# Kernel tuning notes

Measured on AMD Instinct MI355X. Metric: run time of the kernel, lower is better.

## Reference

```python
import jax, jax.numpy as jnp
import numpy as np

N = 30000      # nodes
E = 480000     # edges (avg degree 16)
NF = 4         # n_field
NM = 8         # n_meshfield
H = 128        # hidden_size == latent_size
T = 4          # n_time
DEPTH_MID = 8  # depth-2 middle convs per GCNBlock
EPS = 1e-5     # PyG InstanceNorm eps
DT = 5 * (4.0 / 200)  # = 0.1, hard-coded in forward


def _glorot(k, shape):
    fan_in = shape[-2]
    return (jax.random.uniform(k, shape, jnp.float32, -1.0, 1.0) / np.sqrt(fan_in)).astype(jnp.float32)


def setup_inputs() -> dict:
    key = jax.random.key(0)
    ks = jax.random.split(key, 12)
    inp = {}
    inp['F_0'] = jax.random.normal(ks[0], (N, NF), jnp.float32)
    inp['edge_index'] = jax.random.randint(ks[1], (2, E), 0, N)
    inp['meshfield'] = jax.random.normal(ks[2], (N, NM), jnp.float32)
    inp['n_time'] = T
    # mesh_decriptor GCNBlock params (10 GCNConv layers)
    inp['mesh_W0'] = _glorot(ks[3], (NM, H)); inp['mesh_b0'] = jnp.zeros((H,), jnp.float32)
    inp['mesh_Wh'] = _glorot(ks[4], (DEPTH_MID, H, H)); inp['mesh_bh'] = jnp.zeros((DEPTH_MID, H), jnp.float32)
    inp['mesh_W9'] = _glorot(ks[5], (H, H)); inp['mesh_b9'] = jnp.zeros((H,), jnp.float32)
    # differentiator GCNBlock params; input dim = n_field + latent_size
    din = NF + H
    inp['diff_W0'] = _glorot(ks[6], (din, H)); inp['diff_b0'] = jnp.zeros((H,), jnp.float32)
    inp['diff_Wh'] = _glorot(ks[7], (DEPTH_MID, H, H)); inp['diff_bh'] = jnp.zeros((DEPTH_MID, H), jnp.float32)
    inp['diff_W9'] = _glorot(ks[8], (H, NF)); inp['diff_b9'] = jnp.zeros((NF,), jnp.float32)
    return inp


def _gcn_norm(edge_index, n):
    # PyG GCNConv: add self-loops, sym-normalize D^-1/2 (A+I) D^-1/2
    loops = jnp.arange(n)
    row = jnp.concatenate([edge_index[0], loops])
    col = jnp.concatenate([edge_index[1], loops])
    deg = jax.ops.segment_sum(jnp.ones_like(col, jnp.float32), col, num_segments=n)
    dinv = jnp.where(deg > 0, jax.lax.rsqrt(jnp.maximum(deg, 1.0)), 0.0)
    return row, col, dinv[row] * dinv[col]


def _conv(x, W, b, row, col, enorm, n):
    h = x @ W                                   # [n, out]
    m = h[row] * enorm[:, None]                 # gather + edge normalization
    return jax.ops.segment_sum(m, col, num_segments=n) + b  # scatter-add + bias


def _instance_norm(x):
    # single graph, affine=False: per-channel normalize over nodes
    m = x.mean(axis=0)
    v = x.var(axis=0)
    return (x - m) * jax.lax.rsqrt(v + EPS)


def _gcn_block(x, W0, b0, Wh, bh, W9, b9, row, col, enorm, n):
    x = _conv(x, W0, b0, row, col, enorm, n)
    x = _instance_norm(x)
    def body(c, wb):
        W, b = wb
        return _conv(jax.nn.relu(c), W, b, row, col, enorm, n), None
    x, _ = jax.lax.scan(body, x, (Wh, bh))
    return _conv(x, W9, b9, row, col, enorm, n)


def reference(F_0, edge_index, meshfield, n_time,
              mesh_W0, mesh_b0, mesh_Wh, mesh_bh, mesh_W9, mesh_b9,
              diff_W0, diff_b0, diff_Wh, diff_bh, diff_W9, diff_b9):
    n = F_0.shape[0]
    row, col, enorm = _gcn_norm(edge_index, n)
    mesh = jnp.tanh(_gcn_block(meshfield, mesh_W0, mesh_b0, mesh_Wh, mesh_bh,
                               mesh_W9, mesh_b9, row, col, enorm, n))

    def step(F_cur, _):
        x = jnp.concatenate([F_cur, mesh], axis=1)   # [n, n_field + latent]
        F_dot = jnp.tanh(_gcn_block(x, diff_W0, diff_b0, diff_Wh, diff_bh,
                                    diff_W9, diff_b9, row, col, enorm, n))
        F_next = jnp.tanh(F_cur + F_dot * DT)
        # original: F_current = F_next.detach()
        return jax.lax.stop_gradient(F_next), (F_next, F_dot)

    _, (Fs, F_dots) = jax.lax.scan(step, F_0, None, length=n_time)
    # [T, n, f] -> [n, T, f] to match torch.cat(..., dim=1)
    return jnp.transpose(Fs, (1, 0, 2)), jnp.transpose(F_dots, (1, 0, 2))
```

## Files before the change

### kernel.cpp

```cpp
#include <hip/hip_runtime.h>
#include <math.h>

typedef __attribute__((ext_vector_type(8))) short short8;
typedef __attribute__((ext_vector_type(4))) float f32x4;
typedef unsigned int uint;
typedef unsigned short ushort;

__device__ __forceinline__ ushort f2bf(float f) {
  union { float f; uint u; } v; v.f = f;
  uint u = v.u;
  uint r = (u + 0x7FFFu + ((u >> 16) & 1u)) >> 16;
  return (ushort)r;
}
__device__ __forceinline__ float bflo(uint u) { union { uint u; float f; } v; v.u = u << 16; return v.f; }
__device__ __forceinline__ float bfhi(uint u) { union { uint u; float f; } v; v.u = u & 0xFFFF0000u; return v.f; }
__device__ __forceinline__ uint packbf(float a, float b) { return (uint)f2bf(a) | ((uint)f2bf(b) << 16); }


static __global__ void k_count(const int* __restrict__ col, int* __restrict__ cnt, int E) {
  int e = blockIdx.x * blockDim.x + threadIdx.x;
  if (e < E) atomicAdd(&cnt[col[e]], 1);
}

static __global__ void k_dinv(const int* __restrict__ cnt, float* __restrict__ dinv, int N) {
  int v = blockIdx.x * blockDim.x + threadIdx.x;
  if (v < N) dinv[v] = rsqrtf((float)cnt[v] + 1.0f);
}

static __global__ void k_scan(const int* __restrict__ cnt, int* __restrict__ rowptr, int N) {
  __shared__ int buf[1024];
  __shared__ int carry;
  int t = threadIdx.x;
  if (t == 0) carry = 0;
  __syncthreads();
  for (int base = 0; base < N; base += 1024) {
    int i = base + t;
    int x = (i < N) ? cnt[i] : 0;
    buf[t] = x;
    __syncthreads();
    for (int o = 1; o < 1024; o <<= 1) {
      int val = (t >= o) ? buf[t - o] : 0;
      __syncthreads();
      buf[t] += val;
      __syncthreads();
    }
    int inc = buf[t];
    if (i < N) rowptr[i] = carry + inc - x;
    __syncthreads();
    if (t == 1023) carry += inc;
    __syncthreads();
  }
  if (t == 0) rowptr[N] = carry;
}

static __global__ void k_fill(const int* __restrict__ row, const int* __restrict__ col,
                              const float* __restrict__ dinv, const int* __restrict__ rowptr,
                              int* __restrict__ fillc, int* __restrict__ csr_src,
                              float* __restrict__ csr_w, int E) {
  int e = blockIdx.x * blockDim.x + threadIdx.x;
  if (e >= E) return;
  int s = row[e], d = col[e];
  int pos = rowptr[d] + atomicAdd(&fillc[d], 1);
  csr_src[pos] = s;
  csr_w[pos] = dinv[s] * dinv[d];
}


static __global__ void k_wprep(const float* __restrict__ W, ushort* __restrict__ Wt,
                               int K, int Kpad, int Nc) {
  int l = blockIdx.y;
  int idx = blockIdx.x * 256 + threadIdx.x;
  if (idx >= Nc * Kpad) return;
  int n = idx / Kpad, k = idx - n * Kpad;
  const float* Wl = W + (size_t)l * K * Nc;
  ushort* Wtl = Wt + (size_t)l * Nc * Kpad;
  Wtl[idx] = (k < K) ? f2bf(Wl[(size_t)k * Nc + n]) : (ushort)0;
}


static __global__ __launch_bounds__(256) void k_gemm16(
    const ushort* __restrict__ A, const ushort* __restrict__ Bt,
    ushort* __restrict__ Y, int M, int K) {
  __shared__ ushort As[128 * 40];
  __shared__ ushort Bs[128 * 40];
  const int tid = threadIdx.x;
  const int lane = tid & 63;
  const int wave = tid >> 6;
  const int wr = wave >> 1, wc = wave & 1;
  const int bm = blockIdx.x * 128;
  const int l15 = lane & 15, lk = lane >> 4;
  const int r0 = tid >> 2, o0 = tid & 3;

  f32x4 acc[4][4];
#pragma unroll
  for (int i = 0; i < 4; ++i)
#pragma unroll
    for (int j = 0; j < 4; ++j) acc[i][j] = (f32x4){0.f, 0.f, 0.f, 0.f};

  for (int k0 = 0; k0 < K; k0 += 32) {
    short8 a0 = *(const short8*)(A + (size_t)(bm + r0) * K + k0 + o0 * 8);
    short8 a1 = *(const short8*)(A + (size_t)(bm + r0 + 64) * K + k0 + o0 * 8);
    short8 b0 = *(const short8*)(Bt + (size_t)r0 * K + k0 + o0 * 8);
    short8 b1 = *(const short8*)(Bt + (size_t)(r0 + 64) * K + k0 + o0 * 8);
    __syncthreads();
    *(short8*)(As + r0 * 40 + o0 * 8) = a0;
    *(short8*)(As + (r0 + 64) * 40 + o0 * 8) = a1;
    *(short8*)(Bs + r0 * 40 + o0 * 8) = b0;
    *(short8*)(Bs + (r0 + 64) * 40 + o0 * 8) = b1;
    __syncthreads();
    short8 af[4], bfr[4];
#pragma unroll
    for (int i = 0; i < 4; ++i) {
      af[i]  = *(const short8*)(As + (wr * 64 + i * 16 + l15) * 40 + lk * 8);
      bfr[i] = *(const short8*)(Bs + (wc * 64 + i * 16 + l15) * 40 + lk * 8);
    }
#pragma unroll
    for (int i = 0; i < 4; ++i)
#pragma unroll
      for (int j = 0; j < 4; ++j)
        acc[i][j] = __builtin_amdgcn_mfma_f32_16x16x32_bf16(af[i], bfr[j], acc[i][j], 0, 0, 0);
  }
#pragma unroll
  for (int i = 0; i < 4; ++i) {
#pragma unroll
    for (int r = 0; r < 4; ++r) {
      int row = bm + wr * 64 + i * 16 + lk * 4 + r;
      if (row < M) {
#pragma unroll
        for (int j = 0; j < 4; ++j) {
          int col = wc * 64 + j * 16 + l15;
          Y[(size_t)row * 128 + col] = f2bf(acc[i][j][r]);
        }
      }
    }
  }
}


static __global__ __launch_bounds__(256) void k_gemm_small(
    const ushort* __restrict__ A, const float* __restrict__ W, float* __restrict__ Y, int M) {
  __shared__ float Ws[512];
  int tid = threadIdx.x;
  for (int i = tid; i < 512; i += 256) Ws[i] = W[i];
  __syncthreads();
  int m = blockIdx.x * 256 + tid;
  if (m >= M) return;
  const uint* a = (const uint*)(A + (size_t)m * 128);
  float a0 = 0, a1 = 0, a2 = 0, a3 = 0;
#pragma unroll 8
  for (int k2 = 0; k2 < 64; ++k2) {
    uint u = a[k2];
    float x0 = bflo(u), x1 = bfhi(u);
    const float* w = Ws + k2 * 8;
    a0 += x0 * w[0] + x1 * w[4];
    a1 += x0 * w[1] + x1 * w[5];
    a2 += x0 * w[2] + x1 * w[6];
    a3 += x0 * w[3] + x1 * w[7];
  }
  float* y = Y + (size_t)m * 4;
  y[0] = a0; y[1] = a1; y[2] = a2; y[3] = a3;
}


static __global__ __launch_bounds__(256) void k_agg16(
    const ushort* __restrict__ Hm, const int* __restrict__ rowptr,
    const int* __restrict__ csr_src, const float* __restrict__ csr_w,
    const float* __restrict__ dinv, const float* __restrict__ bias,
    float* __restrict__ outF, int actF,
    ushort* __restrict__ outB, int reluB,
    int N) {
  int node = blockIdx.x * 4 + (threadIdx.x >> 6);
  if (node >= N) return;
  int lane = threadIdx.x & 63;
  const uint* __restrict__ Hu = (const uint*)Hm;
  float dv = dinv[node];
  float w = dv * dv;
  uint su = Hu[(size_t)node * 64 + lane];
  float acc0 = w * bflo(su), acc1 = w * bfhi(su);
  int s = rowptr[node], e = rowptr[node + 1];
  int i = s;
  for (; i + 4 <= e; i += 4) {
    int s0 = csr_src[i], s1 = csr_src[i + 1], s2 = csr_src[i + 2], s3 = csr_src[i + 3];
    float w0 = csr_w[i], w1 = csr_w[i + 1], w2 = csr_w[i + 2], w3 = csr_w[i + 3];
    uint u0 = Hu[(size_t)s0 * 64 + lane];
    uint u1 = Hu[(size_t)s1 * 64 + lane];
    uint u2 = Hu[(size_t)s2 * 64 + lane];
    uint u3 = Hu[(size_t)s3 * 64 + lane];
    acc0 += w0 * bflo(u0) + w1 * bflo(u1) + w2 * bflo(u2) + w3 * bflo(u3);
    acc1 += w0 * bfhi(u0) + w1 * bfhi(u1) + w2 * bfhi(u2) + w3 * bfhi(u3);
  }
  for (; i < e; ++i) {
    int s0 = csr_src[i];
    float w0 = csr_w[i];
    uint u0 = Hu[(size_t)s0 * 64 + lane];
    acc0 += w0 * bflo(u0);
    acc1 += w0 * bfhi(u0);
  }
  float2 bb = *(const float2*)(bias + lane * 2);
  acc0 += bb.x; acc1 += bb.y;
  if (outF) {
    float o0 = acc0, o1 = acc1;
    if (actF == 2) { o0 = tanhf(o0); o1 = tanhf(o1); }
    *(float2*)(outF + (size_t)node * 128 + lane * 2) = make_float2(o0, o1);
  }
  if (outB) {
    float o0 = acc0, o1 = acc1;
    if (reluB) { o0 = fmaxf(o0, 0.f); o1 = fmaxf(o1, 0.f); }
    ((uint*)outB)[(size_t)node * 64 + lane] = packbf(o0, o1);
  }
}


static __global__ void k_agg_f32(const float* __restrict__ Hm, float* __restrict__ Y,
                                 const int* __restrict__ rowptr, const int* __restrict__ csr_src,
                                 const float* __restrict__ csr_w, const float* __restrict__ dinv,
                                 const float* __restrict__ bias, int N, int C) {
  int idx = blockIdx.x * blockDim.x + threadIdx.x;
  if (idx >= N * C) return;
  int v = idx / C, c = idx - v * C;
  float dv = dinv[v];
  float acc = dv * dv * Hm[(size_t)v * C + c];
  int s = rowptr[v], e = rowptr[v + 1];
  for (int i = s; i < e; ++i) acc += csr_w[i] * Hm[(size_t)csr_src[i] * C + c];
  Y[idx] = acc + bias[c];
}


static __global__ __launch_bounds__(256) void k_in_part(const float* __restrict__ X,
                                                        float* __restrict__ acc, int N) {
  int tid = threadIdx.x;
  int c4 = (tid & 31) * 4;
  int rsub = tid >> 5;
  int row0 = blockIdx.x * 512 + rsub;
  int rowEnd = min(blockIdx.x * 512 + 512, N);
  float s0 = 0, s1 = 0, s2 = 0, s3 = 0, q0 = 0, q1 = 0, q2 = 0, q3 = 0;
  for (int r = row0; r < rowEnd; r += 8) {
    float4 v = *(const float4*)(X + (size_t)r * 128 + c4);
    s0 += v.x; s1 += v.y; s2 += v.z; s3 += v.w;
    q0 += v.x * v.x; q1 += v.y * v.y; q2 += v.z * v.z; q3 += v.w * v.w;
  }
  __shared__ float sb[8][132], qb[8][132];
  sb[rsub][c4] = s0; sb[rsub][c4 + 1] = s1; sb[rsub][c4 + 2] = s2; sb[rsub][c4 + 3] = s3;
  qb[rsub][c4] = q0; qb[rsub][c4 + 1] = q1; qb[rsub][c4 + 2] = q2; qb[rsub][c4 + 3] = q3;
  __syncthreads();
  if (tid < 128) {
    float ss = 0, qq = 0;
#pragma unroll
    for (int g = 0; g < 8; ++g) { ss += sb[g][tid]; qq += qb[g][tid]; }
    atomicAdd(&acc[tid], ss);
    atomicAdd(&acc[128 + tid], qq);
  }
}

static __global__ void k_in_fin(const float* __restrict__ acc, float* __restrict__ meanv,
                                float* __restrict__ scalev, int N) {
  int c = threadIdx.x;
  if (c < 128) {
    float m = acc[c] / (float)N;
    float var = acc[128 + c] / (float)N - m * m;
    meanv[c] = m;
    scalev[c] = rsqrtf(var + 1e-5f);
  }
}

static __global__ void k_in_apply(const float* __restrict__ X, const float* __restrict__ meanv,
                                  const float* __restrict__ scalev, ushort* __restrict__ outB, int N) {
  int idx = blockIdx.x * blockDim.x + threadIdx.x;
  if (idx >= N * 64) return;
  int c2 = idx & 63;
  float2 x = *(const float2*)(X + (size_t)idx * 2);
  float2 mm = *(const float2*)(meanv + c2 * 2);
  float2 sc = *(const float2*)(scalev + c2 * 2);
  float o0 = fmaxf((x.x - mm.x) * sc.x, 0.f);
  float o1 = fmaxf((x.y - mm.y) * sc.y, 0.f);
  ((uint*)outB)[idx] = packbf(o0, o1);
}


static __global__ void k_cast_mesh0(const float* __restrict__ MF, ushort* __restrict__ A16, int N) {
  int idx = blockIdx.x * blockDim.x + threadIdx.x;
  if (idx >= N * 16) return;
  int v = idx >> 4, c2 = idx & 15;
  int c = c2 * 2;
  float x0 = 0.f, x1 = 0.f;
  if (c < 8) { x0 = MF[v * 8 + c]; x1 = MF[v * 8 + c + 1]; }
  ((uint*)A16)[idx] = packbf(x0, x1);
}

static __global__ void k_concat16(const float* __restrict__ F, const float* __restrict__ meshL,
                                  ushort* __restrict__ A16, int N) {
  int idx = blockIdx.x * blockDim.x + threadIdx.x;
  if (idx >= N * 80) return;
  int v = idx / 80, c2 = idx - v * 80;
  int c = c2 * 2;
  float x0 = 0.f, x1 = 0.f;
  if (c < 4) { x0 = F[v * 4 + c]; x1 = F[v * 4 + c + 1]; }
  else if (c < 132) { float2 m = *(const float2*)(meshL + (size_t)v * 128 + (c - 4)); x0 = m.x; x1 = m.y; }
  ((uint*)A16)[idx] = packbf(x0, x1);
}

static __global__ void k_copy(const float* __restrict__ A, float* __restrict__ B, int n) {
  int i = blockIdx.x * blockDim.x + threadIdx.x;
  if (i < n) B[i] = A[i];
}

static __global__ void k_step_finish(const float* __restrict__ fdot_pre,
                                     const float* __restrict__ Fcur, float* __restrict__ Fnext,
                                     float* __restrict__ out, int N, int T, int t) {
  int idx = blockIdx.x * blockDim.x + threadIdx.x;
  if (idx >= N * 4) return;
  int v = idx >> 2, f = idx & 3;
  float fd = tanhf(fdot_pre[idx]);
  float fn = tanhf(Fcur[idx] + fd * 0.1f);
  Fnext[idx] = fn;
  out[((size_t)v * T + t) * 4 + f] = fn;
  out[(size_t)N * T * 4 + ((size_t)v * T + t) * 4 + f] = fd;
}


extern "C" void kernel_launch(void* const* d_in, const int* in_sizes, int n_in,
                              void* d_out, int out_size, void* d_ws, size_t ws_size,
                              hipStream_t stream) {
  const float* F0        = (const float*)d_in[0];
  const int*   ei        = (const int*)d_in[1];
  const float* meshfield = (const float*)d_in[2];
  const float* mesh_W0 = (const float*)d_in[4];
  const float* mesh_b0 = (const float*)d_in[5];
  const float* mesh_Wh = (const float*)d_in[6];
  const float* mesh_bh = (const float*)d_in[7];
  const float* mesh_W9 = (const float*)d_in[8];
  const float* mesh_b9 = (const float*)d_in[9];
  const float* diff_W0 = (const float*)d_in[10];
  const float* diff_b0 = (const float*)d_in[11];
  const float* diff_Wh = (const float*)d_in[12];
  const float* diff_bh = (const float*)d_in[13];
  const float* diff_W9 = (const float*)d_in[14];
  const float* diff_b9 = (const float*)d_in[15];

  const int N = in_sizes[0] / 4;
  const int E = in_sizes[1] / 2;
  const int H = in_sizes[5];
  const int T = out_size / (N * 4 * 2);
  const int DEPTH = in_sizes[7] / H;
  const int Mpad = (N + 127) / 128 * 128;
  const int DIN_K = 160;

  const int* erow = ei;
  const int* ecol = ei + E;

  char* p = (char*)d_ws;
  auto alloc = [&](size_t bytes) { char* r = p; p += (bytes + 255) & ~(size_t)255; return r; };
  float* dinv   = (float*)alloc((size_t)N * 4);
  float* X      = (float*)alloc((size_t)N * H * 4);
  float* meshL  = (float*)alloc((size_t)N * H * 4);
  ushort* A16   = (ushort*)alloc((size_t)Mpad * DIN_K * 2);
  ushort* Msg16 = (ushort*)alloc((size_t)Mpad * H * 2);
  float* msg4   = (float*)alloc((size_t)N * 4 * 4);
  float* fdotp  = (float*)alloc((size_t)N * 4 * 4);
  float* fcur0  = (float*)alloc((size_t)N * 4 * 4);
  float* fcur1  = (float*)alloc((size_t)N * 4 * 4);
  float* statac = (float*)alloc(256 * 4);
  float* meanv  = (float*)alloc(128 * 4);
  float* scalev = (float*)alloc(128 * 4);
  ushort* W0t_m = (ushort*)alloc((size_t)128 * 32 * 2);
  ushort* Wht_m = (ushort*)alloc((size_t)DEPTH * 128 * 128 * 2);
  ushort* W9t_m = (ushort*)alloc((size_t)128 * 128 * 2);
  ushort* W0t_d = (ushort*)alloc((size_t)128 * 160 * 2);
  ushort* Wht_d = (ushort*)alloc((size_t)DEPTH * 128 * 128 * 2);
  float* csr_w  = (float*)alloc((size_t)E * 4);
  int* cnt      = (int*)alloc((size_t)N * 4);
  int* rowptr   = (int*)alloc((size_t)(N + 1) * 4);
  int* fillc    = (int*)alloc((size_t)N * 4);
  int* csr_src  = (int*)alloc((size_t)E * 4);

  {
    dim3 g0((128 * 32 + 255) / 256, 1);
    k_wprep<<<g0, 256, 0, stream>>>(mesh_W0, W0t_m, 8, 32, 128);
    dim3 gh((128 * 128 + 255) / 256, DEPTH);
    k_wprep<<<gh, 256, 0, stream>>>(mesh_Wh, Wht_m, 128, 128, 128);
    dim3 g9((128 * 128 + 255) / 256, 1);
    k_wprep<<<g9, 256, 0, stream>>>(mesh_W9, W9t_m, 128, 128, 128);
    dim3 gd((128 * 160 + 255) / 256, 1);
    k_wprep<<<gd, 256, 0, stream>>>(diff_W0, W0t_d, 132, 160, 128);
    k_wprep<<<gh, 256, 0, stream>>>(diff_Wh, Wht_d, 128, 128, 128);
  }

  hipMemsetAsync(cnt, 0, (size_t)N * 4, stream);
  hipMemsetAsync(fillc, 0, (size_t)N * 4, stream);
  k_count<<<(E + 255) / 256, 256, 0, stream>>>(ecol, cnt, E);
  k_dinv<<<(N + 255) / 256, 256, 0, stream>>>(cnt, dinv, N);
  k_scan<<<1, 1024, 0, stream>>>(cnt, rowptr, N);
  k_fill<<<(E + 255) / 256, 256, 0, stream>>>(erow, ecol, dinv, rowptr, fillc, csr_src, csr_w, E);

  auto gemm = [&](const ushort* A, const ushort* Bt, int K) {
    k_gemm16<<<Mpad / 128, 256, 0, stream>>>(A, Bt, Msg16, N, K);
  };
  auto agg = [&](const float* bias, float* outF, int actF, ushort* outB, int reluB) {
    k_agg16<<<(N + 3) / 4, 256, 0, stream>>>(Msg16, rowptr, csr_src, csr_w, dinv, bias,
                                             outF, actF, outB, reluB, N);
  };
  auto instnorm = [&]() {
    hipMemsetAsync(statac, 0, 256 * 4, stream);
    k_in_part<<<(N + 511) / 512, 256, 0, stream>>>(X, statac, N);
    k_in_fin<<<1, 128, 0, stream>>>(statac, meanv, scalev, N);
    k_in_apply<<<(N * 64 + 255) / 256, 256, 0, stream>>>(X, meanv, scalev, A16, N);
  };

  k_cast_mesh0<<<(N * 16 + 255) / 256, 256, 0, stream>>>(meshfield, A16, N);
  gemm(A16, W0t_m, 32);
  agg(mesh_b0, X, 0, nullptr, 0);
  instnorm();
  for (int i = 0; i < DEPTH; ++i) {
    gemm(A16, Wht_m + (size_t)i * 128 * 128, 128);
    agg(mesh_bh + (size_t)i * H, nullptr, 0, A16, (i < DEPTH - 1) ? 1 : 0);
  }
  gemm(A16, W9t_m, 128);
  agg(mesh_b9, meshL, 2 , nullptr, 0);

  k_copy<<<(N * 4 + 255) / 256, 256, 0, stream>>>(F0, fcur0, N * 4);
  float* fc = fcur0;
  float* fn = fcur1;
  float* out = (float*)d_out;

  for (int t = 0; t < T; ++t) {
    k_concat16<<<(N * 80 + 255) / 256, 256, 0, stream>>>(fc, meshL, A16, N);
    gemm(A16, W0t_d, DIN_K);
    agg(diff_b0, X, 0, nullptr, 0);
    instnorm();
    for (int i = 0; i < DEPTH; ++i) {
      gemm(A16, Wht_d + (size_t)i * 128 * 128, 128);
      agg(diff_bh + (size_t)i * H, nullptr, 0, A16, (i < DEPTH - 1) ? 1 : 0);
    }
    k_gemm_small<<<(N + 255) / 256, 256, 0, stream>>>(A16, diff_W9, msg4, N);
    k_agg_f32<<<(N * 4 + 255) / 256, 256, 0, stream>>>(msg4, fdotp, rowptr, csr_src, csr_w,
                                                       dinv, diff_b9, N, 4);
    k_step_finish<<<(N * 4 + 255) / 256, 256, 0, stream>>>(fdotp, fc, fn, out, N, T, t);
    float* tmp = fc; fc = fn; fn = tmp;
  }
}
```

Before: 2.092 ms.

## Fuse neighbor aggregation into GEMM conv kernel using aggregate-then-transform order

Each GCN conv layer becomes one kernel. It first aggregates neighbor features (A·X) for a 128-node tile into LDS, then multiplies by the weight with MFMA and applies bias and activation in the epilogue. This relies on (A·X)·W = A·(X·W) and removes the intermediate message buffer round trip and one launch per layer. The cost is a serial gather phase per block with low parallelism: only 235 blocks, each wave handling 32 nodes in sequence. Gathering 160-wide inputs for the first diff layer also costs more. The single-block scan now uses shuffle-based chunked scanning. Instance-norm statistics are reduced through per-block partials instead of atomics, which drops a memset.

```diff
diff --git a/kernel.cpp b/kernel.cpp
--- a/kernel.cpp
+++ b/kernel.cpp
@@ -27,30 +27,39 @@
   if (v < N) dinv[v] = rsqrtf((float)cnt[v] + 1.0f);
 }
 
-static __global__ void k_scan(const int* __restrict__ cnt, int* __restrict__ rowptr, int N) {
-  __shared__ int buf[1024];
-  __shared__ int carry;
-  int t = threadIdx.x;
-  if (t == 0) carry = 0;
+static __global__ __launch_bounds__(1024) void k_scan(const int* __restrict__ cnt,
+                                                      int* __restrict__ rowptr, int N) {
+  const int t = threadIdx.x;
+  const int per = (N + 1023) / 1024;
+  int lo = t * per, hi = min(lo + per, N);
+  if (lo > N) lo = N;
+  if (hi < lo) hi = lo;
+  int sum = 0;
+  for (int i = lo; i < hi; ++i) sum += cnt[i];
+  int lane = t & 63, w = t >> 6;
+  int v = sum;
+#pragma unroll
+  for (int d = 1; d < 64; d <<= 1) {
+    int u = __shfl_up(v, d, 64);
+    if (lane >= d) v += u;
+  }
+  __shared__ int wsum[16];
+  if (lane == 63) wsum[w] = v;
   __syncthreads();
-  for (int base = 0; base < N; base += 1024) {
-    int i = base + t;
-    int x = (i < N) ? cnt[i] : 0;
-    buf[t] = x;
-    __syncthreads();
-    for (int o = 1; o < 1024; o <<= 1) {
-      int val = (t >= o) ? buf[t - o] : 0;
-      __syncthreads();
-      buf[t] += val;
-      __syncthreads();
-    }
-    int inc = buf[t];
-    if (i < N) rowptr[i] = carry + inc - x;
-    __syncthreads();
-    if (t == 1023) carry += inc;
-    __syncthreads();
-  }
-  if (t == 0) rowptr[N] = carry;
+  if (t < 16) {
+    int x = wsum[t];
+#pragma unroll
+    for (int d = 1; d < 16; d <<= 1) {
+      int u = __shfl_up(x, d, 64);
+      if (t >= d) x += u;
+    }
+    wsum[t] = x;
+  }
+  __syncthreads();
+  int base = (w ? wsum[w - 1] : 0) + v - sum;
+  int run = base;
+  for (int i = lo; i < hi; ++i) { rowptr[i] = run; run += cnt[i]; }
+  if (t == 1023) rowptr[N] = run;
 }
 
 static __global__ void k_fill(const int* __restrict__ row, const int* __restrict__ col,
@@ -78,41 +87,120 @@
 }
 
 
-static __global__ __launch_bounds__(256) void k_gemm16(
-    const ushort* __restrict__ A, const ushort* __restrict__ Bt,
-    ushort* __restrict__ Y, int M, int K) {
-  __shared__ ushort As[128 * 40];
-  __shared__ ushort Bs[128 * 40];
+template <int KPAD>
+static __global__ __launch_bounds__(256) void k_conv(
+    const ushort* __restrict__ Xin, const ushort* __restrict__ Bt,
+    const int* __restrict__ rowptr, const int* __restrict__ csr_src,
+    const float* __restrict__ csr_w, const float* __restrict__ dinv,
+    const float* __restrict__ bias,
+    float* __restrict__ outF, int actF,
+    ushort* __restrict__ outB, int reluB,
+    int N) {
+  constexpr int KU = KPAD / 2;
+  constexpr int STR = KPAD + 8;
+  constexpr int STRU = STR / 2;
+  constexpr int K8 = KPAD / 8;
+  __shared__ ushort As[128 * STR];
+  __shared__ ushort Bs[128 * STR];
   const int tid = threadIdx.x;
   const int lane = tid & 63;
   const int wave = tid >> 6;
+  const int bm = blockIdx.x * 128;
+
+  for (int ii = tid; ii < 128 * K8; ii += 256) {
+    int r = ii / K8, o = ii - r * K8;
+    *(short8*)(Bs + r * STR + o * 8) = *(const short8*)(Bt + (size_t)r * KPAD + o * 8);
+  }
+
+  const uint* __restrict__ Xu = (const uint*)Xin;
+  uint* AsU = (uint*)As;
+
+  if constexpr (KU <= 64) {
+    constexpr int NPI = 64 / KU;
+    const int c = lane % KU;
+    const int sub = lane / KU;
+    for (int j = wave * 32 + sub; j < (wave + 1) * 32; j += NPI) {
+      int nd = bm + j;
+      float a0 = 0.f, a1 = 0.f;
+      if (nd < N) {
+        float dv = dinv[nd];
+        float wsl = dv * dv;
+        uint u = Xu[(size_t)nd * KU + c];
+        a0 = wsl * bflo(u);
+        a1 = wsl * bfhi(u);
+        int s = rowptr[nd], e = rowptr[nd + 1];
+        int i = s;
+        for (; i + 4 <= e; i += 4) {
+          int s0 = csr_src[i], s1 = csr_src[i + 1], s2 = csr_src[i + 2], s3 = csr_src[i + 3];
+          float w0 = csr_w[i], w1 = csr_w[i + 1], w2 = csr_w[i + 2], w3 = csr_w[i + 3];
+          uint u0 = Xu[(size_t)s0 * KU + c];
+          uint u1 = Xu[(size_t)s1 * KU + c];
+          uint u2 = Xu[(size_t)s2 * KU + c];
+          uint u3 = Xu[(size_t)s3 * KU + c];
+          a0 += w0 * bflo(u0) + w1 * bflo(u1) + w2 * bflo(u2) + w3 * bflo(u3);
+          a1 += w0 * bfhi(u0) + w1 * bfhi(u1) + w2 * bfhi(u2) + w3 * bfhi(u3);
+        }
+        for (; i < e; ++i) {
+          float w0 = csr_w[i];
+          uint u0 = Xu[(size_t)csr_src[i] * KU + c];
+          a0 += w0 * bflo(u0);
+          a1 += w0 * bfhi(u0);
+        }
+      }
+      AsU[j * STRU + c] = packbf(a0, a1);
+    }
+  } else {
+    for (int j = wave * 32; j < (wave + 1) * 32; ++j) {
+      int nd = bm + j;
+      float a0 = 0.f, a1 = 0.f, b0 = 0.f, b1 = 0.f;
+      const int c0 = lane, c1 = lane + 64;
+      const bool has2 = lane < (KU - 64);
+      if (nd < N) {
+        float dv = dinv[nd];
+        float wsl = dv * dv;
+        uint u = Xu[(size_t)nd * KU + c0];
+        a0 = wsl * bflo(u);
+        a1 = wsl * bfhi(u);
+        if (has2) {
+          uint u2 = Xu[(size_t)nd * KU + c1];
+          b0 = wsl * bflo(u2);
+          b1 = wsl * bfhi(u2);
+        }
+        int s = rowptr[nd], e = rowptr[nd + 1];
+        for (int i = s; i < e; ++i) {
+          int sv = csr_src[i];
+          float w0 = csr_w[i];
+          uint u0 = Xu[(size_t)sv * KU + c0];
+          a0 += w0 * bflo(u0);
+          a1 += w0 * bfhi(u0);
+          if (has2) {
+            uint u2 = Xu[(size_t)sv * KU + c1];
+            b0 += w0 * bflo(u2);
+            b1 += w0 * bfhi(u2);
+          }
+        }
+      }
+      AsU[j * STRU + c0] = packbf(a0, a1);
+      if (has2) AsU[j * STRU + c1] = packbf(b0, b1);
+    }
+  }
+  __syncthreads();
+
   const int wr = wave >> 1, wc = wave & 1;
-  const int bm = blockIdx.x * 128;
   const int l15 = lane & 15, lk = lane >> 4;
-  const int r0 = tid >> 2, o0 = tid & 3;
-
   f32x4 acc[4][4];
 #pragma unroll
   for (int i = 0; i < 4; ++i)
 #pragma unroll
     for (int j = 0; j < 4; ++j) acc[i][j] = (f32x4){0.f, 0.f, 0.f, 0.f};
 
-  for (int k0 = 0; k0 < K; k0 += 32) {
-    short8 a0 = *(const short8*)(A + (size_t)(bm + r0) * K + k0 + o0 * 8);
-    short8 a1 = *(const short8*)(A + (size_t)(bm + r0 + 64) * K + k0 + o0 * 8);
-    short8 b0 = *(const short8*)(Bt + (size_t)r0 * K + k0 + o0 * 8);
-    short8 b1 = *(const short8*)(Bt + (size_t)(r0 + 64) * K + k0 + o0 * 8);
-    __syncthreads();
-    *(short8*)(As + r0 * 40 + o0 * 8) = a0;
-    *(short8*)(As + (r0 + 64) * 40 + o0 * 8) = a1;
-    *(short8*)(Bs + r0 * 40 + o0 * 8) = b0;
-    *(short8*)(Bs + (r0 + 64) * 40 + o0 * 8) = b1;
-    __syncthreads();
+#pragma unroll
+  for (int k0 = 0; k0 < KPAD; k0 += 32) {
     short8 af[4], bfr[4];
 #pragma unroll
     for (int i = 0; i < 4; ++i) {
-      af[i]  = *(const short8*)(As + (wr * 64 + i * 16 + l15) * 40 + lk * 8);
-      bfr[i] = *(const short8*)(Bs + (wc * 64 + i * 16 + l15) * 40 + lk * 8);
+      af[i]  = *(const short8*)(As + (wr * 64 + i * 16 + l15) * STR + k0 + lk * 8);
+      bfr[i] = *(const short8*)(Bs + (wc * 64 + i * 16 + l15) * STR + k0 + lk * 8);
     }
 #pragma unroll
     for (int i = 0; i < 4; ++i)
@@ -120,16 +208,22 @@
       for (int j = 0; j < 4; ++j)
         acc[i][j] = __builtin_amdgcn_mfma_f32_16x16x32_bf16(af[i], bfr[j], acc[i][j], 0, 0, 0);
   }
+
 #pragma unroll
   for (int i = 0; i < 4; ++i) {
 #pragma unroll
     for (int r = 0; r < 4; ++r) {
       int row = bm + wr * 64 + i * 16 + lk * 4 + r;
-      if (row < M) {
-#pragma unroll
-        for (int j = 0; j < 4; ++j) {
-          int col = wc * 64 + j * 16 + l15;
-          Y[(size_t)row * 128 + col] = f2bf(acc[i][j][r]);
+      if (row >= N) continue;
+#pragma unroll
+      for (int j = 0; j < 4; ++j) {
+        int col = wc * 64 + j * 16 + l15;
+        float v = acc[i][j][r] + bias[col];
+        if (outF) {
+          outF[(size_t)row * 128 + col] = (actF == 2) ? tanhf(v) : v;
+        }
+        if (outB) {
+          outB[(size_t)row * 128 + col] = f2bf(reluB ? fmaxf(v, 0.f) : v);
         }
       }
     }
@@ -162,55 +256,6 @@
 }
 
 
-static __global__ __launch_bounds__(256) void k_agg16(
-    const ushort* __restrict__ Hm, const int* __restrict__ rowptr,
-    const int* __restrict__ csr_src, const float* __restrict__ csr_w,
-    const float* __restrict__ dinv, const float* __restrict__ bias,
-    float* __restrict__ outF, int actF,
-    ushort* __restrict__ outB, int reluB,
-    int N) {
-  int node = blockIdx.x * 4 + (threadIdx.x >> 6);
-  if (node >= N) return;
-  int lane = threadIdx.x & 63;
-  const uint* __restrict__ Hu = (const uint*)Hm;
-  float dv = dinv[node];
-  float w = dv * dv;
-  uint su = Hu[(size_t)node * 64 + lane];
-  float acc0 = w * bflo(su), acc1 = w * bfhi(su);
-  int s = rowptr[node], e = rowptr[node + 1];
-  int i = s;
-  for (; i + 4 <= e; i += 4) {
-    int s0 = csr_src[i], s1 = csr_src[i + 1], s2 = csr_src[i + 2], s3 = csr_src[i + 3];
-    float w0 = csr_w[i], w1 = csr_w[i + 1], w2 = csr_w[i + 2], w3 = csr_w[i + 3];
-    uint u0 = Hu[(size_t)s0 * 64 + lane];
-    uint u1 = Hu[(size_t)s1 * 64 + lane];
-    uint u2 = Hu[(size_t)s2 * 64 + lane];
-    uint u3 = Hu[(size_t)s3 * 64 + lane];
-    acc0 += w0 * bflo(u0) + w1 * bflo(u1) + w2 * bflo(u2) + w3 * bflo(u3);
-    acc1 += w0 * bfhi(u0) + w1 * bfhi(u1) + w2 * bfhi(u2) + w3 * bfhi(u3);
-  }
-  for (; i < e; ++i) {
-    int s0 = csr_src[i];
-    float w0 = csr_w[i];
-    uint u0 = Hu[(size_t)s0 * 64 + lane];
-    acc0 += w0 * bflo(u0);
-    acc1 += w0 * bfhi(u0);
-  }
-  float2 bb = *(const float2*)(bias + lane * 2);
-  acc0 += bb.x; acc1 += bb.y;
-  if (outF) {
-    float o0 = acc0, o1 = acc1;
-    if (actF == 2) { o0 = tanhf(o0); o1 = tanhf(o1); }
-    *(float2*)(outF + (size_t)node * 128 + lane * 2) = make_float2(o0, o1);
-  }
-  if (outB) {
-    float o0 = acc0, o1 = acc1;
-    if (reluB) { o0 = fmaxf(o0, 0.f); o1 = fmaxf(o1, 0.f); }
-    ((uint*)outB)[(size_t)node * 64 + lane] = packbf(o0, o1);
-  }
-}
-
-
 static __global__ void k_agg_f32(const float* __restrict__ Hm, float* __restrict__ Y,
                                  const int* __restrict__ rowptr, const int* __restrict__ csr_src,
                                  const float* __restrict__ csr_w, const float* __restrict__ dinv,
@@ -227,7 +272,7 @@
 
 
 static __global__ __launch_bounds__(256) void k_in_part(const float* __restrict__ X,
-                                                        float* __restrict__ acc, int N) {
+                                                        float* __restrict__ partial, int N) {
   int tid = threadIdx.x;
   int c4 = (tid & 31) * 4;
   int rsub = tid >> 5;
@@ -247,20 +292,24 @@
     float ss = 0, qq = 0;
 #pragma unroll
     for (int g = 0; g < 8; ++g) { ss += sb[g][tid]; qq += qb[g][tid]; }
-    atomicAdd(&acc[tid], ss);
-    atomicAdd(&acc[128 + tid], qq);
-  }
-}
-
-static __global__ void k_in_fin(const float* __restrict__ acc, float* __restrict__ meanv,
-                                float* __restrict__ scalev, int N) {
+    partial[(size_t)blockIdx.x * 256 + tid] = ss;
+    partial[(size_t)blockIdx.x * 256 + 128 + tid] = qq;
+  }
+}
+
+static __global__ void k_in_fin(const float* __restrict__ partial, int NB,
+                                float* __restrict__ meanv, float* __restrict__ scalev, int N) {
   int c = threadIdx.x;
-  if (c < 128) {
-    float m = acc[c] / (float)N;
-    float var = acc[128 + c] / (float)N - m * m;
-    meanv[c] = m;
-    scalev[c] = rsqrtf(var + 1e-5f);
-  }
+  if (c >= 128) return;
+  float s = 0, q = 0;
+  for (int b = 0; b < NB; ++b) {
+    s += partial[(size_t)b * 256 + c];
+    q += partial[(size_t)b * 256 + 128 + c];
+  }
+  float m = s / (float)N;
+  float var = q / (float)N - m * m;
+  meanv[c] = m;
+  scalev[c] = rsqrtf(var + 1e-5f);
 }
 
 static __global__ void k_in_apply(const float* __restrict__ X, const float* __restrict__ meanv,
@@ -277,18 +326,18 @@
 }
 
 
-static __global__ void k_cast_mesh0(const float* __restrict__ MF, ushort* __restrict__ A16, int N) {
+static __global__ void k_cast_mesh0(const float* __restrict__ MF, ushort* __restrict__ C32, int N) {
   int idx = blockIdx.x * blockDim.x + threadIdx.x;
   if (idx >= N * 16) return;
   int v = idx >> 4, c2 = idx & 15;
   int c = c2 * 2;
   float x0 = 0.f, x1 = 0.f;
   if (c < 8) { x0 = MF[v * 8 + c]; x1 = MF[v * 8 + c + 1]; }
-  ((uint*)A16)[idx] = packbf(x0, x1);
+  ((uint*)C32)[idx] = packbf(x0, x1);
 }
 
 static __global__ void k_concat16(const float* __restrict__ F, const float* __restrict__ meshL,
-                                  ushort* __restrict__ A16, int N) {
+                                  ushort* __restrict__ C160, int N) {
   int idx = blockIdx.x * blockDim.x + threadIdx.x;
   if (idx >= N * 80) return;
   int v = idx / 80, c2 = idx - v * 80;
@@ -296,7 +345,7 @@
   float x0 = 0.f, x1 = 0.f;
   if (c < 4) { x0 = F[v * 4 + c]; x1 = F[v * 4 + c + 1]; }
   else if (c < 132) { float2 m = *(const float2*)(meshL + (size_t)v * 128 + (c - 4)); x0 = m.x; x1 = m.y; }
-  ((uint*)A16)[idx] = packbf(x0, x1);
+  ((uint*)C160)[idx] = packbf(x0, x1);
 }
 
 static __global__ void k_copy(const float* __restrict__ A, float* __restrict__ B, int n) {
@@ -343,7 +392,7 @@
   const int T = out_size / (N * 4 * 2);
   const int DEPTH = in_sizes[7] / H;
   const int Mpad = (N + 127) / 128 * 128;
-  const int DIN_K = 160;
+  const int NB_IN = (N + 511) / 512;
 
   const int* erow = ei;
   const int* ecol = ei + E;
@@ -353,13 +402,15 @@
   float* dinv   = (float*)alloc((size_t)N * 4);
   float* X      = (float*)alloc((size_t)N * H * 4);
   float* meshL  = (float*)alloc((size_t)N * H * 4);
-  ushort* A16   = (ushort*)alloc((size_t)Mpad * DIN_K * 2);
-  ushort* Msg16 = (ushort*)alloc((size_t)Mpad * H * 2);
+  ushort* C32   = (ushort*)alloc((size_t)Mpad * 32 * 2);
+  ushort* C160  = (ushort*)alloc((size_t)Mpad * 160 * 2);
+  ushort* X16a  = (ushort*)alloc((size_t)Mpad * 128 * 2);
+  ushort* X16b  = (ushort*)alloc((size_t)Mpad * 128 * 2);
   float* msg4   = (float*)alloc((size_t)N * 4 * 4);
   float* fdotp  = (float*)alloc((size_t)N * 4 * 4);
   float* fcur0  = (float*)alloc((size_t)N * 4 * 4);
   float* fcur1  = (float*)alloc((size_t)N * 4 * 4);
-  float* statac = (float*)alloc(256 * 4);
+  float* partial= (float*)alloc((size_t)NB_IN * 256 * 4);
   float* meanv  = (float*)alloc(128 * 4);
   float* scalev = (float*)alloc(128 * 4);
   ushort* W0t_m = (ushort*)alloc((size_t)128 * 32 * 2);
@@ -392,30 +443,38 @@
   k_scan<<<1, 1024, 0, stream>>>(cnt, rowptr, N);
   k_fill<<<(E + 255) / 256, 256, 0, stream>>>(erow, ecol, dinv, rowptr, fillc, csr_src, csr_w, E);
 
-  auto gemm = [&](const ushort* A, const ushort* Bt, int K) {
-    k_gemm16<<<Mpad / 128, 256, 0, stream>>>(A, Bt, Msg16, N, K);
+  const int GCONV = Mpad / 128;
+
+  auto conv32 = [&](const ushort* Xin, const ushort* Bt, const float* b,
+                    float* oF, int aF, ushort* oB, int rB) {
+    k_conv<32><<<GCONV, 256, 0, stream>>>(Xin, Bt, rowptr, csr_src, csr_w, dinv, b, oF, aF, oB, rB, N);
   };
-  auto agg = [&](const float* bias, float* outF, int actF, ushort* outB, int reluB) {
-    k_agg16<<<(N + 3) / 4, 256, 0, stream>>>(Msg16, rowptr, csr_src, csr_w, dinv, bias,
-                                             outF, actF, outB, reluB, N);
+  auto conv128 = [&](const ushort* Xin, const ushort* Bt, const float* b,
+                     float* oF, int aF, ushort* oB, int rB) {
+    k_conv<128><<<GCONV, 256, 0, stream>>>(Xin, Bt, rowptr, csr_src, csr_w, dinv, b, oF, aF, oB, rB, N);
+  };
+  auto conv160 = [&](const ushort* Xin, const ushort* Bt, const float* b,
+                     float* oF, int aF, ushort* oB, int rB) {
+    k_conv<160><<<GCONV, 256, 0, stream>>>(Xin, Bt, rowptr, csr_src, csr_w, dinv, b, oF, aF, oB, rB, N);
   };
   auto instnorm = [&]() {
-    hipMemsetAsync(statac, 0, 256 * 4, stream);
-    k_in_part<<<(N + 511) / 512, 256, 0, stream>>>(X, statac, N);
-    k_in_fin<<<1, 128, 0, stream>>>(statac, meanv, scalev, N);
-    k_in_apply<<<(N * 64 + 255) / 256, 256, 0, stream>>>(X, meanv, scalev, A16, N);
+    k_in_part<<<NB_IN, 256, 0, stream>>>(X, partial, N);
+    k_in_fin<<<1, 128, 0, stream>>>(partial, NB_IN, meanv, scalev, N);
+    k_in_apply<<<(N * 64 + 255) / 256, 256, 0, stream>>>(X, meanv, scalev, X16a, N);
   };
 
-  k_cast_mesh0<<<(N * 16 + 255) / 256, 256, 0, stream>>>(meshfield, A16, N);
-  gemm(A16, W0t_m, 32);
-  agg(mesh_b0, X, 0, nullptr, 0);
+  k_cast_mesh0<<<(N * 16 + 255) / 256, 256, 0, stream>>>(meshfield, C32, N);
+  conv32(C32, W0t_m, mesh_b0, X, 0, nullptr, 0);
   instnorm();
-  for (int i = 0; i < DEPTH; ++i) {
-    gemm(A16, Wht_m + (size_t)i * 128 * 128, 128);
-    agg(mesh_bh + (size_t)i * H, nullptr, 0, A16, (i < DEPTH - 1) ? 1 : 0);
-  }
-  gemm(A16, W9t_m, 128);
-  agg(mesh_b9, meshL, 2 , nullptr, 0);
+  {
+    ushort* cur = X16a; ushort* nxt = X16b;
+    for (int i = 0; i < DEPTH; ++i) {
+      conv128(cur, Wht_m + (size_t)i * 128 * 128, mesh_bh + (size_t)i * H,
+              nullptr, 0, nxt, (i < DEPTH - 1) ? 1 : 0);
+      ushort* tmp = cur; cur = nxt; nxt = tmp;
+    }
+    conv128(cur, W9t_m, mesh_b9, meshL, 2 , nullptr, 0);
+  }
 
   k_copy<<<(N * 4 + 255) / 256, 256, 0, stream>>>(F0, fcur0, N * 4);
   float* fc = fcur0;
@@ -423,15 +482,16 @@
   float* out = (float*)d_out;
 
   for (int t = 0; t < T; ++t) {
-    k_concat16<<<(N * 80 + 255) / 256, 256, 0, stream>>>(fc, meshL, A16, N);
-    gemm(A16, W0t_d, DIN_K);
-    agg(diff_b0, X, 0, nullptr, 0);
+    k_concat16<<<(N * 80 + 255) / 256, 256, 0, stream>>>(fc, meshL, C160, N);
+    conv160(C160, W0t_d, diff_b0, X, 0, nullptr, 0);
     instnorm();
+    ushort* cur = X16a; ushort* nxt = X16b;
     for (int i = 0; i < DEPTH; ++i) {
-      gemm(A16, Wht_d + (size_t)i * 128 * 128, 128);
-      agg(diff_bh + (size_t)i * H, nullptr, 0, A16, (i < DEPTH - 1) ? 1 : 0);
-    }
-    k_gemm_small<<<(N + 255) / 256, 256, 0, stream>>>(A16, diff_W9, msg4, N);
+      conv128(cur, Wht_d + (size_t)i * 128 * 128, diff_bh + (size_t)i * H,
+              nullptr, 0, nxt, (i < DEPTH - 1) ? 1 : 0);
+      ushort* tmp = cur; cur = nxt; nxt = tmp;
+    }
+    k_gemm_small<<<(N + 255) / 256, 256, 0, stream>>>(cur, diff_W9, msg4, N);
     k_agg_f32<<<(N * 4 + 255) / 256, 256, 0, stream>>>(msg4, fdotp, rowptr, csr_src, csr_w,
                                                        dinv, diff_b9, N, 4);
     k_step_finish<<<(N * 4 + 255) / 256, 256, 0, stream>>>(fdotp, fc, fn, out, N, T, t);
```

Result: slower. 6.456 ms (+208.6%).
